# Optimization experiments

Measured on AMD Instinct MI355X. Metric: run time of the kernel, lower is better.

## Reference

```python
import jax, jax.numpy as jnp
import numpy as np

NUM_NODES = 100000
NUM_EDGES = 1600000
DIM = 64
NUM_LAYERS = 3


def setup_inputs() -> dict:
    key = jax.random.key(0)
    k1, k2 = jax.random.split(key)
    x = jax.random.normal(k1, (NUM_NODES, DIM), dtype=jnp.float32)
    adj_t = jax.random.randint(k2, (2, NUM_EDGES), 0, NUM_NODES, dtype=jnp.int64)
    return {"x": x, "adj_t": adj_t}


def reference(x, adj_t):
    n = x.shape[0]
    # undirected -> add reversed edges (adj_t_is_undirected=True path)
    edge_index = jnp.concatenate([adj_t, adj_t[::-1]], axis=1)  # [2, 2E]
    row, col = edge_index[0], edge_index[1]
    edge_weight = jnp.ones((row.shape[0],), dtype=x.dtype)
    # gcn_norm: D^-0.5 A D^-0.5 (degree computed by scatter over col)
    deg = jax.ops.segment_sum(edge_weight, col, num_segments=n)
    deg_inv_sqrt = jnp.where(deg > 0, jax.lax.rsqrt(deg), 0.0).astype(x.dtype)
    w = deg_inv_sqrt[row] * edge_weight * deg_inv_sqrt[col]  # [2E]
    outs = [x]
    for _ in range(NUM_LAYERS):
        # gather -> scale -> scatter_add (SpMM)
        msgs = w[:, None] * x[row]                     # [2E, D]
        x = jax.ops.segment_sum(msgs, col, num_segments=n)  # [N, D]
        outs.append(x)
    return jnp.mean(jnp.stack(outs), axis=0)
```

## Files before the change

### kernel.cpp

```cpp
#include <hip/hip_runtime.h>

#define DIM 64
#define SCAN_B 256
#define BKT_SHIFT 7
#define BKT_G 128
#define NBLK 256

__device__ inline float blo(unsigned p) { return __uint_as_float(p << 16); }
__device__ inline float bhi(unsigned p) { return __uint_as_float(p & 0xffff0000u); }
__device__ inline unsigned bpack(float x, float y) {
    unsigned ux = __float_as_uint(x);
    unsigned uy = __float_as_uint(y);
    ux += 0x7fffu + ((ux >> 16) & 1u);
    uy += 0x7fffu + ((uy >> 16) & 1u);
    return (ux >> 16) | (uy & 0xffff0000u);
}

__global__ void hist_kernel(const int* __restrict__ adj, int E,
                            int* __restrict__ hist, int NB) {
    extern __shared__ int lh[];
    for (int g = threadIdx.x; g < NB; g += blockDim.x) lh[g] = 0;
    __syncthreads();
    for (int e = blockIdx.x * blockDim.x + threadIdx.x; e < E;
         e += NBLK * blockDim.x) {
        int a = adj[e];
        int b = adj[E + e];
        atomicAdd(&lh[a >> BKT_SHIFT], 1);
        atomicAdd(&lh[b >> BKT_SHIFT], 1);
    }
    __syncthreads();
    for (int g = threadIdx.x; g < NB; g += blockDim.x)
        hist[g * NBLK + blockIdx.x] = lh[g];
}

__global__ void scan_block_kernel(const int* __restrict__ src, int n,
                                  int* __restrict__ dst,
                                  int* __restrict__ blocksums) {
    __shared__ int tmp[SCAN_B];
    int i = blockIdx.x * SCAN_B + threadIdx.x;
    int v = (i < n) ? src[i] : 0;
    tmp[threadIdx.x] = v;
    __syncthreads();
    for (int off = 1; off < SCAN_B; off <<= 1) {
        int t = (threadIdx.x >= off) ? tmp[threadIdx.x - off] : 0;
        __syncthreads();
        tmp[threadIdx.x] += t;
        __syncthreads();
    }
    if (i < n) dst[i] = tmp[threadIdx.x] - v;
    if (threadIdx.x == SCAN_B - 1) blocksums[blockIdx.x] = tmp[SCAN_B - 1];
}

__global__ void scan_sums_kernel(int* __restrict__ blocksums, int nb) {
    __shared__ int tmp[1024];
    int v = (threadIdx.x < nb) ? blocksums[threadIdx.x] : 0;
    tmp[threadIdx.x] = v;
    __syncthreads();
    for (int off = 1; off < 1024; off <<= 1) {
        int t = (threadIdx.x >= off) ? tmp[threadIdx.x - off] : 0;
        __syncthreads();
        tmp[threadIdx.x] += t;
        __syncthreads();
    }
    if (threadIdx.x < nb) blocksums[threadIdx.x] = tmp[threadIdx.x] - v;
}

__global__ void scan_add_kernel(int* __restrict__ dst,
                                const int* __restrict__ blocksums,
                                int n, int total) {
    int i = blockIdx.x * blockDim.x + threadIdx.x;
    if (i < n) dst[i] += blocksums[i / SCAN_B];
    if (i == n) dst[n] = total;
}

__global__ void place_kernel(const int* __restrict__ adj, int E,
                             const int* __restrict__ hist_s,
                             unsigned* __restrict__ pairs, int NB) {
    extern __shared__ int cur[];
    for (int g = threadIdx.x; g < NB; g += blockDim.x)
        cur[g] = hist_s[g * NBLK + blockIdx.x];
    __syncthreads();
    for (int e = blockIdx.x * blockDim.x + threadIdx.x; e < E;
         e += NBLK * blockDim.x) {
        int a = adj[e];
        int b = adj[E + e];
        int pb = atomicAdd(&cur[b >> BKT_SHIFT], 1);
        pairs[pb] = ((unsigned)(b & (BKT_G - 1)) << 17) | (unsigned)a;
        int pa = atomicAdd(&cur[a >> BKT_SHIFT], 1);
        pairs[pa] = ((unsigned)(a & (BKT_G - 1)) << 17) | (unsigned)b;
    }
}

__global__ void pass2_build_kernel(const unsigned* __restrict__ pairs,
                                   const int* __restrict__ hist_s,
                                   int* __restrict__ csr_src,
                                   int* __restrict__ row_ptr,
                                   int* __restrict__ deg,
                                   float* __restrict__ dinv,
                                   int N, int total_adj) {
    __shared__ int cnt[BKT_G];
    __shared__ int pre[BKT_G];
    __shared__ int cur[BKT_G];
    int g = blockIdx.x;
    int base = g << BKT_SHIFT;
    int off = hist_s[(size_t)g * NBLK];
    int offn = (g + 1 < gridDim.x) ? hist_s[(size_t)(g + 1) * NBLK] : total_adj;
    int m = offn - off;
    if (threadIdx.x < BKT_G) cnt[threadIdx.x] = 0;
    __syncthreads();
    for (int i = threadIdx.x; i < m; i += blockDim.x)
        atomicAdd(&cnt[pairs[off + i] >> 17], 1);
    __syncthreads();
    if (threadIdx.x < BKT_G) pre[threadIdx.x] = cnt[threadIdx.x];
    __syncthreads();
    for (int o = 1; o < BKT_G; o <<= 1) {
        int t = 0;
        if (threadIdx.x < BKT_G && threadIdx.x >= o) t = pre[threadIdx.x - o];
        __syncthreads();
        if (threadIdx.x < BKT_G) pre[threadIdx.x] += t;
        __syncthreads();
    }
    if (threadIdx.x < BKT_G) {
        int v = base + threadIdx.x;
        if (v < N) {
            int c = cnt[threadIdx.x];
            int start = off + pre[threadIdx.x] - c;
            row_ptr[v] = start;
            deg[v] = c;
            dinv[v] = (c > 0) ? rsqrtf((float)c) : 0.0f;
            cur[threadIdx.x] = start;
        }
    }
    if (g == gridDim.x - 1 && threadIdx.x == 0) row_ptr[N] = total_adj;
    __syncthreads();
    for (int i = threadIdx.x; i < m; i += blockDim.x) {
        unsigned p = pairs[off + i];
        int dl  = (int)(p >> 17);
        int src = (int)(p & 0x1ffffu);
        int pos = atomicAdd(&cur[dl], 1);
        csr_src[pos] = src;
    }
}

__global__ void init_xs_kernel(const float4* __restrict__ x,
                               const float* __restrict__ dinv,
                               uint4* __restrict__ xs0, int N) {
    int t = blockIdx.x * blockDim.x + threadIdx.x;
    int v = t >> 3, sub = t & 7;
    if (v >= N) return;
    float4 xa = x[(size_t)v * 16 + sub * 2];
    float4 xb = x[(size_t)v * 16 + sub * 2 + 1];
    float di = dinv[v];
    uint4 o;
    o.x = bpack(di * xa.x, di * xa.y);
    o.y = bpack(di * xa.z, di * xa.w);
    o.z = bpack(di * xb.x, di * xb.y);
    o.w = bpack(di * xb.z, di * xb.w);
    xs0[(size_t)v * 8 + sub] = o;
}

__global__ void spmm_bf16_kernel(const int* __restrict__ row_ptr,
                                 const int* __restrict__ csr_src,
                                 const float* __restrict__ dinv,
                                 const uint4* __restrict__ xs_in,
                                 uint4* __restrict__ xs_out, int N) {
    int t = blockIdx.x * blockDim.x + threadIdx.x;
    int v = t >> 5;
    if (v >= N) return;
    int half = threadIdx.x & 31;
    int nb = half >> 3, sub = half & 7;
    int beg = row_ptr[v];
    int end = row_ptr[v + 1];
    float a0 = 0, a1 = 0, a2 = 0, a3 = 0, a4 = 0, a5 = 0, a6 = 0, a7 = 0;
    for (int j0 = beg; j0 < end; j0 += 4) {
        int idx = j0 + nb;
        if (idx < end) {
            int s = csr_src[idx];
            uint4 p = xs_in[(size_t)s * 8 + sub];
            a0 += blo(p.x); a1 += bhi(p.x);
            a2 += blo(p.y); a3 += bhi(p.y);
            a4 += blo(p.z); a5 += bhi(p.z);
            a6 += blo(p.w); a7 += bhi(p.w);
        }
    }
    a0 += __shfl_xor(a0, 8);  a0 += __shfl_xor(a0, 16);
    a1 += __shfl_xor(a1, 8);  a1 += __shfl_xor(a1, 16);
    a2 += __shfl_xor(a2, 8);  a2 += __shfl_xor(a2, 16);
    a3 += __shfl_xor(a3, 8);  a3 += __shfl_xor(a3, 16);
    a4 += __shfl_xor(a4, 8);  a4 += __shfl_xor(a4, 16);
    a5 += __shfl_xor(a5, 8);  a5 += __shfl_xor(a5, 16);
    a6 += __shfl_xor(a6, 8);  a6 += __shfl_xor(a6, 16);
    a7 += __shfl_xor(a7, 8);  a7 += __shfl_xor(a7, 16);
    if (nb == 0) {
        float di = dinv[v];
        float d2 = di * di;
        uint4 o;
        o.x = bpack(d2 * a0, d2 * a1);
        o.y = bpack(d2 * a2, d2 * a3);
        o.z = bpack(d2 * a4, d2 * a5);
        o.w = bpack(d2 * a6, d2 * a7);
        xs_out[(size_t)v * 8 + sub] = o;
    }
}

__global__ void final_kernel(const float4* __restrict__ x,
                             const int* __restrict__ deg,
                             const uint4* __restrict__ xs1,
                             const uint4* __restrict__ xs2,
                             const uint4* __restrict__ xs3,
                             float4* __restrict__ out, int N) {
    int t = blockIdx.x * blockDim.x + threadIdx.x;
    int v = t >> 3, sub = t & 7;
    if (v >= N) return;
    size_t idx = (size_t)v * 8 + sub;
    uint4 p1 = xs1[idx], p2 = xs2[idx], p3 = xs3[idx];
    float rs = sqrtf((float)deg[v]);
    float s0 = blo(p1.x) + blo(p2.x) + blo(p3.x);
    float s1 = bhi(p1.x) + bhi(p2.x) + bhi(p3.x);
    float s2 = blo(p1.y) + blo(p2.y) + blo(p3.y);
    float s3 = bhi(p1.y) + bhi(p2.y) + bhi(p3.y);
    float s4 = blo(p1.z) + blo(p2.z) + blo(p3.z);
    float s5 = bhi(p1.z) + bhi(p2.z) + bhi(p3.z);
    float s6 = blo(p1.w) + blo(p2.w) + blo(p3.w);
    float s7 = bhi(p1.w) + bhi(p2.w) + bhi(p3.w);
    float4 xa = x[(size_t)v * 16 + sub * 2];
    float4 xb = x[(size_t)v * 16 + sub * 2 + 1];
    float4 oa, ob;
    oa.x = 0.25f * (xa.x + rs * s0);
    oa.y = 0.25f * (xa.y + rs * s1);
    oa.z = 0.25f * (xa.z + rs * s2);
    oa.w = 0.25f * (xa.w + rs * s3);
    ob.x = 0.25f * (xb.x + rs * s4);
    ob.y = 0.25f * (xb.y + rs * s5);
    ob.z = 0.25f * (xb.z + rs * s6);
    ob.w = 0.25f * (xb.w + rs * s7);
    out[(size_t)v * 16 + sub * 2]     = oa;
    out[(size_t)v * 16 + sub * 2 + 1] = ob;
}

extern "C" void kernel_launch(void* const* d_in, const int* in_sizes, int n_in,
                              void* d_out, int out_size, void* d_ws, size_t ws_size,
                              hipStream_t stream) {
    const float* x = (const float*)d_in[0];
    const int* adj = (const int*)d_in[1];
    float* out     = (float*)d_out;

    const int total_adj = in_sizes[1];
    const int E = total_adj / 2;
    const int N = in_sizes[0] / DIM;
    const int NB = (N + BKT_G - 1) / BKT_G;
    const int nhist = NB * NBLK;

    size_t BUF = (size_t)total_adj * 4;
    size_t xsb = (size_t)N * 32 * 4;
    if (xsb > BUF) BUF = xsb;
    BUF = (BUF + 255) & ~(size_t)255;

    char* ws = (char*)d_ws;
    int*      deg     = (int*)(ws);
    float*    dinv    = (float*)(ws + (size_t)512 * 1024);
    int*      row_ptr = (int*)(ws + (size_t)1024 * 1024);
    int*      bsums   = (int*)(ws + (size_t)1536 * 1024);
    int*      hist    = (int*)(ws + (size_t)1600 * 1024);
    int*      hist_s  = (int*)(ws + (size_t)2432 * 1024);
    char*     big     = ws + (size_t)3264 * 1024;
    int*      csr_src = (int*)(big);
    unsigned* pairs   = (unsigned*)(big + BUF);
    uint4*    xs0     = (uint4*)(big + BUF);
    uint4*    xs1     = (uint4*)(big + 2 * BUF);
    uint4*    xs2     = (uint4*)(big + 3 * BUF);
    uint4*    xs3     = (uint4*)(big + 4 * BUF);

    const int B = 256;

    hist_kernel<<<NBLK, B, NB * sizeof(int), stream>>>(adj, E, hist, NB);

    const int nscan2 = (nhist + SCAN_B - 1) / SCAN_B;
    scan_block_kernel<<<nscan2, SCAN_B, 0, stream>>>(hist, nhist, hist_s, bsums);
    scan_sums_kernel<<<1, 1024, 0, stream>>>(bsums, nscan2);
    scan_add_kernel<<<(nhist + 1 + B - 1) / B, B, 0, stream>>>(hist_s, bsums, nhist, total_adj);

    place_kernel<<<NBLK, B, NB * sizeof(int), stream>>>(adj, E, hist_s, pairs, NB);

    pass2_build_kernel<<<NB, B, 0, stream>>>(pairs, hist_s, csr_src, row_ptr,
                                             deg, dinv, N, total_adj);

    const int nblocks8 = (int)(((long long)N * 8 + B - 1) / B);
    init_xs_kernel<<<nblocks8, B, 0, stream>>>((const float4*)x, dinv, xs0, N);

    const int nblocks32 = (int)(((long long)N * 32 + B - 1) / B);
    spmm_bf16_kernel<<<nblocks32, B, 0, stream>>>(row_ptr, csr_src, dinv, xs0, xs1, N);
    spmm_bf16_kernel<<<nblocks32, B, 0, stream>>>(row_ptr, csr_src, dinv, xs1, xs2, N);
    spmm_bf16_kernel<<<nblocks32, B, 0, stream>>>(row_ptr, csr_src, dinv, xs2, xs3, N);

    final_kernel<<<nblocks8, B, 0, stream>>>((const float4*)x, deg, xs1, xs2, xs3,
                                             (float4*)out, N);
}
```

Before: 345.7 us.

## Fuse xs0 init into CSR build, prefetch indices in SpMM, widen hist blocks

The separate init_xs kernel is folded into pass2_build: each bucket block scales and packs its own nodes' features into a new xs0 buffer, using dinv held in shared memory. This saves a launch and a dinv reload. The SpMM loop now handles two neighbors per lane per iteration and software-prefetches the next indices, using masked loads to add memory-level parallelism. The hist and place kernels run with 1024-thread blocks. The extra xs0 buffer needs workspace at offset 5*BUF, so it relies on the workspace being large enough.

```diff
diff --git a/kernel.cpp b/kernel.cpp
--- a/kernel.cpp
+++ b/kernel.cpp
@@ -5,6 +5,7 @@
 #define BKT_SHIFT 7
 #define BKT_G 128
 #define NBLK 256
+#define HIST_B 1024
 
 __device__ inline float blo(unsigned p) { return __uint_as_float(p << 16); }
 __device__ inline float bhi(unsigned p) { return __uint_as_float(p & 0xffff0000u); }
@@ -16,8 +17,9 @@
     return (ux >> 16) | (uy & 0xffff0000u);
 }
 
-__global__ void hist_kernel(const int* __restrict__ adj, int E,
-                            int* __restrict__ hist, int NB) {
+__global__ __launch_bounds__(HIST_B)
+void hist_kernel(const int* __restrict__ adj, int E,
+                 int* __restrict__ hist, int NB) {
     extern __shared__ int lh[];
     for (int g = threadIdx.x; g < NB; g += blockDim.x) lh[g] = 0;
     __syncthreads();
@@ -73,9 +75,10 @@
     if (i == n) dst[n] = total;
 }
 
-__global__ void place_kernel(const int* __restrict__ adj, int E,
-                             const int* __restrict__ hist_s,
-                             unsigned* __restrict__ pairs, int NB) {
+__global__ __launch_bounds__(HIST_B)
+void place_kernel(const int* __restrict__ adj, int E,
+                  const int* __restrict__ hist_s,
+                  unsigned* __restrict__ pairs, int NB) {
     extern __shared__ int cur[];
     for (int g = threadIdx.x; g < NB; g += blockDim.x)
         cur[g] = hist_s[g * NBLK + blockIdx.x];
@@ -93,14 +96,17 @@
 
 __global__ void pass2_build_kernel(const unsigned* __restrict__ pairs,
                                    const int* __restrict__ hist_s,
+                                   const float4* __restrict__ x,
                                    int* __restrict__ csr_src,
                                    int* __restrict__ row_ptr,
                                    int* __restrict__ deg,
                                    float* __restrict__ dinv,
+                                   uint4* __restrict__ xs0,
                                    int N, int total_adj) {
     __shared__ int cnt[BKT_G];
     __shared__ int pre[BKT_G];
     __shared__ int cur[BKT_G];
+    __shared__ float dv[BKT_G];
     int g = blockIdx.x;
     int base = g << BKT_SHIFT;
     int off = hist_s[(size_t)g * NBLK];
@@ -125,9 +131,11 @@
         if (v < N) {
             int c = cnt[threadIdx.x];
             int start = off + pre[threadIdx.x] - c;
+            float di = (c > 0) ? rsqrtf((float)c) : 0.0f;
             row_ptr[v] = start;
             deg[v] = c;
-            dinv[v] = (c > 0) ? rsqrtf((float)c) : 0.0f;
+            dinv[v] = di;
+            dv[threadIdx.x] = di;
             cur[threadIdx.x] = start;
         }
     }
@@ -140,23 +148,21 @@
         int pos = atomicAdd(&cur[dl], 1);
         csr_src[pos] = src;
     }
-}
-
-__global__ void init_xs_kernel(const float4* __restrict__ x,
-                               const float* __restrict__ dinv,
-                               uint4* __restrict__ xs0, int N) {
-    int t = blockIdx.x * blockDim.x + threadIdx.x;
-    int v = t >> 3, sub = t & 7;
-    if (v >= N) return;
-    float4 xa = x[(size_t)v * 16 + sub * 2];
-    float4 xb = x[(size_t)v * 16 + sub * 2 + 1];
-    float di = dinv[v];
-    uint4 o;
-    o.x = bpack(di * xa.x, di * xa.y);
-    o.y = bpack(di * xa.z, di * xa.w);
-    o.z = bpack(di * xb.x, di * xb.y);
-    o.w = bpack(di * xb.z, di * xb.w);
-    xs0[(size_t)v * 8 + sub] = o;
+    for (int w = threadIdx.x; w < BKT_G * 8; w += blockDim.x) {
+        int vl = w >> 3, sub = w & 7;
+        int v = base + vl;
+        if (v < N) {
+            float di = dv[vl];
+            float4 xa = x[(size_t)v * 16 + sub * 2];
+            float4 xb = x[(size_t)v * 16 + sub * 2 + 1];
+            uint4 o;
+            o.x = bpack(di * xa.x, di * xa.y);
+            o.y = bpack(di * xa.z, di * xa.w);
+            o.z = bpack(di * xb.x, di * xb.y);
+            o.w = bpack(di * xb.z, di * xb.w);
+            xs0[(size_t)v * 8 + sub] = o;
+        }
+    }
 }
 
 __global__ void spmm_bf16_kernel(const int* __restrict__ row_ptr,
@@ -172,16 +178,26 @@
     int beg = row_ptr[v];
     int end = row_ptr[v + 1];
     float a0 = 0, a1 = 0, a2 = 0, a3 = 0, a4 = 0, a5 = 0, a6 = 0, a7 = 0;
-    for (int j0 = beg; j0 < end; j0 += 4) {
-        int idx = j0 + nb;
-        if (idx < end) {
-            int s = csr_src[idx];
-            uint4 p = xs_in[(size_t)s * 8 + sub];
-            a0 += blo(p.x); a1 += bhi(p.x);
-            a2 += blo(p.y); a3 += bhi(p.y);
-            a4 += blo(p.z); a5 += bhi(p.z);
-            a6 += blo(p.w); a7 += bhi(p.w);
-        }
+    int i0 = beg + nb, i1 = beg + nb + 4;
+    int s0 = (i0 < end) ? csr_src[i0] : -1;
+    int s1 = (i1 < end) ? csr_src[i1] : -1;
+    for (int j = beg; j < end; j += 8) {
+        int ni0 = j + 8 + nb, ni1 = j + 12 + nb;
+        int t0 = (ni0 < end) ? csr_src[ni0] : -1;
+        int t1 = (ni1 < end) ? csr_src[ni1] : -1;
+        uint4 p0 = xs_in[(size_t)(s0 >= 0 ? s0 : 0) * 8 + sub];
+        uint4 p1 = xs_in[(size_t)(s1 >= 0 ? s1 : 0) * 8 + sub];
+        float m0 = (s0 >= 0) ? 1.0f : 0.0f;
+        float m1 = (s1 >= 0) ? 1.0f : 0.0f;
+        a0 += m0 * blo(p0.x); a1 += m0 * bhi(p0.x);
+        a2 += m0 * blo(p0.y); a3 += m0 * bhi(p0.y);
+        a4 += m0 * blo(p0.z); a5 += m0 * bhi(p0.z);
+        a6 += m0 * blo(p0.w); a7 += m0 * bhi(p0.w);
+        a0 += m1 * blo(p1.x); a1 += m1 * bhi(p1.x);
+        a2 += m1 * blo(p1.y); a3 += m1 * bhi(p1.y);
+        a4 += m1 * blo(p1.z); a5 += m1 * bhi(p1.z);
+        a6 += m1 * blo(p1.w); a7 += m1 * bhi(p1.w);
+        s0 = t0; s1 = t1;
     }
     a0 += __shfl_xor(a0, 8);  a0 += __shfl_xor(a0, 16);
     a1 += __shfl_xor(a1, 8);  a1 += __shfl_xor(a1, 16);
@@ -270,29 +286,29 @@
     uint4*    xs1     = (uint4*)(big + 2 * BUF);
     uint4*    xs2     = (uint4*)(big + 3 * BUF);
     uint4*    xs3     = (uint4*)(big + 4 * BUF);
+    uint4*    xs0_s   = (uint4*)(big + 5 * BUF);
 
     const int B = 256;
 
-    hist_kernel<<<NBLK, B, NB * sizeof(int), stream>>>(adj, E, hist, NB);
+    hist_kernel<<<NBLK, HIST_B, NB * sizeof(int), stream>>>(adj, E, hist, NB);
 
     const int nscan2 = (nhist + SCAN_B - 1) / SCAN_B;
     scan_block_kernel<<<nscan2, SCAN_B, 0, stream>>>(hist, nhist, hist_s, bsums);
     scan_sums_kernel<<<1, 1024, 0, stream>>>(bsums, nscan2);
     scan_add_kernel<<<(nhist + 1 + B - 1) / B, B, 0, stream>>>(hist_s, bsums, nhist, total_adj);
 
-    place_kernel<<<NBLK, B, NB * sizeof(int), stream>>>(adj, E, hist_s, pairs, NB);
-
-    pass2_build_kernel<<<NB, B, 0, stream>>>(pairs, hist_s, csr_src, row_ptr,
-                                             deg, dinv, N, total_adj);
-
-    const int nblocks8 = (int)(((long long)N * 8 + B - 1) / B);
-    init_xs_kernel<<<nblocks8, B, 0, stream>>>((const float4*)x, dinv, xs0, N);
+    place_kernel<<<NBLK, HIST_B, NB * sizeof(int), stream>>>(adj, E, hist_s, pairs, NB);
+
+    pass2_build_kernel<<<NB, B, 0, stream>>>(pairs, hist_s, (const float4*)x,
+                                             csr_src, row_ptr, deg, dinv,
+                                             xs0_s, N, total_adj);
 
     const int nblocks32 = (int)(((long long)N * 32 + B - 1) / B);
-    spmm_bf16_kernel<<<nblocks32, B, 0, stream>>>(row_ptr, csr_src, dinv, xs0, xs1, N);
+    spmm_bf16_kernel<<<nblocks32, B, 0, stream>>>(row_ptr, csr_src, dinv, xs0_s, xs1, N);
     spmm_bf16_kernel<<<nblocks32, B, 0, stream>>>(row_ptr, csr_src, dinv, xs1, xs2, N);
     spmm_bf16_kernel<<<nblocks32, B, 0, stream>>>(row_ptr, csr_src, dinv, xs2, xs3, N);
 
+    const int nblocks8 = (int)(((long long)N * 8 + B - 1) / B);
     final_kernel<<<nblocks8, B, 0, stream>>>((const float4*)x, deg, xs1, xs2, xs3,
                                              (float4*)out, N);
 }
```

Result: faster. 302.2 us (-12.6%).
